# Kernel tuning notes

Hardware: AMD Instinct MI355X
Metric: run time of the kernel (lower is better)

The kernel has to match this reference:

```python
import jax, jax.numpy as jnp
import numpy as np

K = 4
TEMP = 34.0
KS = 3
PAD = 1
STRIDE = 1


def setup_inputs() -> dict:
    key = jax.random.key(0)
    k0, k1, k2, k3, k4, k5 = jax.random.split(key, 6)
    B, C, H, W = 32, 256, 56, 56
    OC = 256
    HID = int(C * 0.25) + 1  # 65
    x = jax.random.normal(k0, (B, C, H, W), jnp.float32)
    # kaiming-ish scales for the 1x1 attention convs (treated as matmuls)
    w_fc1 = jax.random.normal(k1, (HID, C), jnp.float32) * np.float32(np.sqrt(2.0 / C))
    w_fc2 = jax.random.normal(k2, (K, HID), jnp.float32) * np.float32(np.sqrt(2.0 / HID))
    b_fc2 = jnp.zeros((K,), jnp.float32)
    # positive step sizes for numerical sanity (torch inits randn then overwrites at init_state)
    alpha = jax.random.uniform(k3, (K, 1), jnp.float32, minval=0.05, maxval=1.0)
    weight = jax.random.normal(k4, (K, OC, C, KS, KS), jnp.float32) * 0.05
    bias_w = jax.random.normal(k5, (K, OC), jnp.float32) * 0.01
    return dict(x=x, w_fc1=w_fc1, w_fc2=w_fc2, b_fc2=b_fc2, alpha=alpha,
                weight=weight, bias_w=bias_w)


def _round_ste(v):
    # round_pass: forward round, backward identity
    return v + jax.lax.stop_gradient(jnp.round(v) - v)


def _lsq_quant(w2d, alpha):
    # Faithful to the torch LSQQuantizer forward (eval path): divide by per-row
    # alpha, clamp ONLY scalar elements [0,0],[1,0],[2,0] (as the torch code does),
    # then straight-through round and rescale. grad_scale copies into .data and
    # therefore has no effect on values or the autograd graph.
    d = w2d / alpha  # (K, M)
    d = d.at[0, 0].set(jnp.clip(d[0, 0], -2.0, 1.0))   # 2-bit range
    d = d.at[1, 0].set(jnp.clip(d[1, 0], -4.0, 3.0))   # 3-bit range
    d = d.at[2, 0].set(jnp.clip(d[2, 0], -8.0, 7.0))   # 4-bit range
    return _round_ste(d) * alpha


def reference(x, w_fc1, w_fc2, b_fc2, alpha, weight, bias_w):
    B, C, H, W = x.shape
    Kk, OC = bias_w.shape
    # attention2d: global avg pool -> 1x1 conv -> relu -> 1x1 conv (+bias)
    pooled = x.mean(axis=(2, 3))                     # (B, C)
    h = jax.nn.relu(pooled @ w_fc1.T)                # (B, HID)
    raw = h @ w_fc2.T + b_fc2                        # (B, K)
    # gradient_approximation: forward = one-hot(argmax), backward = softmax(x/T)
    soft = jax.nn.softmax(raw / TEMP, axis=1)
    hard = jax.nn.one_hot(jnp.argmax(raw, axis=1), Kk, dtype=raw.dtype)
    attn = soft + jax.lax.stop_gradient(hard - soft)  # (B, K)
    # LSQ-quantize flattened expert weights, then per-sample aggregation
    wq = _lsq_quant(weight.reshape(Kk, -1), alpha)   # (K, OC*C*KS*KS)
    agg_w = (attn @ wq).reshape(B, OC, C, KS, KS)    # per-sample kernels
    agg_b = attn @ bias_w                            # (B, OC)
    # per-sample conv2d (equivalent to the groups=batch trick)
    def conv1(xb, wb):
        return jax.lax.conv_general_dilated(
            xb[None], wb, (STRIDE, STRIDE), [(PAD, PAD), (PAD, PAD)],
            dimension_numbers=('NCHW', 'OIHW', 'NCHW'))[0]
    out = jax.vmap(conv1)(x, agg_w) + agg_b[:, :, None, None]  # (B, OC, H, W)
    return (out, raw)
```

## Files before the change

kernel.cpp:

```cpp
#include <hip/hip_runtime.h>
#include <hip/hip_bf16.h>

typedef __attribute__((ext_vector_type(8))) short short8;
typedef __attribute__((ext_vector_type(16))) float f32x16;

#define XPAD_OFF   0u
#define WQ_OFF     55115776u
#define POOL_OFF   59834368u
#define IDX_OFF    59867136u

__device__ __forceinline__ void gl_lds16(const void* g, void* l) {
  __builtin_amdgcn_global_load_lds(
      (const __attribute__((address_space(1))) unsigned int*)g,
      (__attribute__((address_space(3))) unsigned int*)l, 16, 0, 0);
}

__global__ __launch_bounds__(128) void fc_argmax_kernel(
    const float* __restrict__ pooled, const float* __restrict__ w_fc1,
    const float* __restrict__ w_fc2, const float* __restrict__ b_fc2,
    float* __restrict__ raw_out, int* __restrict__ idx) {
  __shared__ float h[65];
  __shared__ float raws[4];
  const int b = blockIdx.x, t = threadIdx.x;
  if (t < 65) {
    float s = 0.f;
    const float* pb = pooled + b * 256;
    const float* wr = w_fc1 + t * 256;
    for (int c = 0; c < 256; ++c) s += pb[c] * wr[c];
    s *= (1.0f / 3136.0f);
    h[t] = s > 0.f ? s : 0.f;
  }
  __syncthreads();
  if (t < 4) {
    float s = b_fc2[t];
    const float* wr = w_fc2 + t * 65;
    for (int j = 0; j < 65; ++j) s += h[j] * wr[j];
    raws[t] = s;
    raw_out[b * 4 + t] = s;
  }
  __syncthreads();
  if (t == 0) {
    int best = 0; float bv = raws[0];
    for (int k = 1; k < 4; ++k) if (raws[k] > bv) { bv = raws[k]; best = k; }
    idx[b] = best;
  }
}

__global__ __launch_bounds__(256) void quant_kernel(
    const float* __restrict__ weight, const float* __restrict__ alpha,
    __hip_bfloat16* __restrict__ Wq) {
  const unsigned d = blockIdx.x * 256u + threadIdx.x;
  const unsigned cl   = d & 7u;
  const unsigned g    = d >> 3;
  const unsigned lane = g & 63u;
  const unsigned u    = g >> 6;
  const unsigned low  = u & 63u;
  const unsigned s      = low & 1u;
  const unsigned octile = (low >> 1) & 1u;
  const unsigned wm     = (low >> 2) & 1u;
  const unsigned cbh    = (low >> 3) & 7u;
  const unsigned t6   = u >> 6;
  const unsigned tap  = t6 % 9u;
  const unsigned q    = t6 / 9u;
  const unsigned ot   = q & 1u;
  const unsigned k    = q >> 1;
  const unsigned oc = ot * 128u + wm * 64u + octile * 32u + (lane & 31u);
  const unsigned ch = cbh * 32u + s * 16u + (lane >> 5) * 8u + cl;
  const float a = alpha[k];
  float v = weight[(size_t)k * 589824u + oc * 2304u + ch * 9u + tap] / a;
  if (oc == 0u && ch == 0u && tap == 0u) {
    if (k == 0u)      v = fminf(fmaxf(v, -2.f), 1.f);
    else if (k == 1u) v = fminf(fmaxf(v, -4.f), 3.f);
    else if (k == 2u) v = fminf(fmaxf(v, -8.f), 7.f);
  }
  Wq[d] = __float2bfloat16(rintf(v) * a);
}

__global__ __launch_bounds__(256) void padx_kernel(const float* __restrict__ x,
                                                   __hip_bfloat16* __restrict__ Xpad,
                                                   float* __restrict__ pooled) {
  __shared__ float T[56 * 132];
  const int yp = blockIdx.x;
  const int c0 = blockIdx.y * 128;
  const int b  = blockIdx.z;
  const int tid = threadIdx.x;
  __hip_bfloat16* orow = Xpad + ((size_t)(b * 58 + yp) * 58) * 256 + c0;
  const short8 zero8 = (short8){0, 0, 0, 0, 0, 0, 0, 0};
  const bool rowin = (yp >= 1 && yp <= 56);
  if (rowin) {
    const float* xbase = x + (((size_t)b * 256 + c0) * 56 + (yp - 1)) * 56;
    for (int i = tid; i < 128 * 56; i += 256) {
      const int cl = i / 56, px = i - cl * 56;
      T[px * 132 + cl] = xbase[cl * 3136 + px];
    }
    __syncthreads();
    if (tid < 128) {
      float s = 0.f;
      for (int px = 0; px < 56; ++px) s += T[px * 132 + tid];
      atomicAdd(pooled + b * 256 + c0 + tid, s);
    }
    for (int i = tid; i < 896; i += 256) {
      const int px = i >> 4, cg = (i & 15) * 8;
      union { short8 v; __hip_bfloat16 e[8]; } u;
      #pragma unroll
      for (int r = 0; r < 8; ++r) u.e[r] = __float2bfloat16(T[px * 132 + cg + r]);
      *(short8*)&orow[(px + 1) * 256 + cg] = u.v;
    }
    for (int i = tid; i < 32; i += 256) {
      const int cg = (i & 15) * 8;
      const int xp = (i >> 4) ? 57 : 0;
      *(short8*)&orow[xp * 256 + cg] = zero8;
    }
  } else {
    for (int i = tid; i < 58 * 16; i += 256) {
      const int xp = i >> 4, cg = (i & 15) * 8;
      *(short8*)&orow[xp * 256 + cg] = zero8;
    }
  }
}

__global__ __launch_bounds__(256, 2) void conv_kernel(
    const __hip_bfloat16* __restrict__ Xpad, const __hip_bfloat16* __restrict__ Wq,
    const int* __restrict__ idx, const float* __restrict__ bias_w,
    float* __restrict__ out) {
  __shared__ __attribute__((aligned(16))) __hip_bfloat16 Xs[22784];

  const int tid = threadIdx.x;
  const int lane = tid & 63;
  const int w = tid >> 6;
  const int wm = w & 1;
  const int wn = w >> 1;

  const int pt = blockIdx.x;
  const int ot = blockIdx.y;
  const int b = blockIdx.z;
  const int Y0 = pt * 4;
  const int OC0 = ot * 128;
  const int kb = idx[b];

  const __hip_bfloat16* xb = Xpad + (size_t)b * (58 * 58 * 256);
  const short8* W0 = (const short8*)Wq + (size_t)(kb * 2 + ot) * 36864;

  f32x16 acc[2][4];
  #pragma unroll
  for (int i = 0; i < 2; ++i)
    #pragma unroll
    for (int j = 0; j < 4; ++j)
      acc[i][j] = (f32x16){0,0,0,0,0,0,0,0,0,0,0,0,0,0,0,0};

  const int nlo = lane & 31;
  const int khalf = lane >> 5;

  auto stageseg = [&](int cbn, int bufsel, int k) {
    int sidx = k * 64 + lane;
    int p = sidx >> 2;
    if (p > 347) p = 347;
    const int gsel = (sidx & 3) ^ ((p >> 1) & 3);
    const int r = p / 58, xc = p - r * 58;
    gl_lds16(xb + (((Y0 + r) * 58 + xc) * 256 + cbn * 32 + gsel * 8),
             (char*)Xs + bufsel * 22784 + k * 1024);
  };

  for (int k = w; k < 22; k += 4) stageseg(0, 0, k);
  __syncthreads();

  short8 afr[3][4];
  #pragma unroll
  for (int oc2 = 0; oc2 < 2; ++oc2)
    #pragma unroll
    for (int s2 = 0; s2 < 2; ++s2) {
      afr[0][oc2 * 2 + s2] = W0[0 * 4096 + 0 * 512 + wm * 256 + oc2 * 128 + s2 * 64 + lane];
      afr[1][oc2 * 2 + s2] = W0[1 * 4096 + 0 * 512 + wm * 256 + oc2 * 128 + s2 * 64 + lane];
    }

  for (int cbh = 0; cbh < 8; ++cbh) {
    const __hip_bfloat16* cur = Xs + (cbh & 1) * 11392;
    const int nb = (cbh + 1) & 1;

    #pragma unroll
    for (int t = 0; t < 9; ++t) {
      const int dy = t / 3, dx = t - dy * 3;
      if (cbh < 7) {
        if (t < 5) stageseg(cbh + 1, nb, w + 4 * t);
        else if (t == 5 && w < 2) stageseg(cbh + 1, nb, w + 20);
      }
      if (cbh < 7 || t < 7) {
        const int tap2 = (t + 2) % 9, cb2 = cbh + (t + 2) / 9;
        #pragma unroll
        for (int oc2 = 0; oc2 < 2; ++oc2)
          #pragma unroll
          for (int s2 = 0; s2 < 2; ++s2)
            afr[(t + 2) % 3][oc2 * 2 + s2] =
                W0[tap2 * 4096 + cb2 * 512 + wm * 256 + oc2 * 128 + s2 * 64 + lane];
      }
      #pragma unroll
      for (int s = 0; s < 2; ++s) {
        #pragma unroll
        for (int j = 0; j < 4; ++j) {
          const int row = wn * 2 + (j >> 1) + dy;
          const int col = (j & 1) * 32 + nlo + dx;
          const int p = row * 58 + col;
          const int slot = p * 4 + ((s * 2 + khalf) ^ ((p >> 1) & 3));
          const short8 bfr = *(const short8*)&cur[slot * 8];
          #pragma unroll
          for (int i = 0; i < 2; ++i)
            acc[i][j] = __builtin_amdgcn_mfma_f32_32x32x16_bf16(
                afr[t % 3][i * 2 + s], bfr, acc[i][j], 0, 0, 0);
        }
      }
    }
    __syncthreads();
  }

  const float* biasb = bias_w + kb * 256;
  #pragma unroll
  for (int i = 0; i < 2; ++i) {
    #pragma unroll
    for (int j = 0; j < 4; ++j) {
      const int xcol = (j & 1) * 32 + nlo;
      if (xcol < 56) {
        const int y = Y0 + wn * 2 + (j >> 1);
        #pragma unroll
        for (int reg = 0; reg < 16; ++reg) {
          const int row = (reg & 3) + 8 * (reg >> 2) + 4 * khalf;
          const int oc = OC0 + wm * 64 + i * 32 + row;
          out[(((size_t)b * 256 + oc) * 56 + y) * 56 + xcol] =
              acc[i][j][reg] + biasb[oc];
        }
      }
    }
  }
}

extern "C" void kernel_launch(void* const* d_in, const int* in_sizes, int n_in,
                              void* d_out, int out_size, void* d_ws, size_t ws_size,
                              hipStream_t stream) {
  const float* x      = (const float*)d_in[0];
  const float* w_fc1  = (const float*)d_in[1];
  const float* w_fc2  = (const float*)d_in[2];
  const float* b_fc2  = (const float*)d_in[3];
  const float* alpha  = (const float*)d_in[4];
  const float* weight = (const float*)d_in[5];
  const float* bias_w = (const float*)d_in[6];

  float* out = (float*)d_out;
  float* raw_out = out + (size_t)32 * 256 * 56 * 56;

  char* ws = (char*)d_ws;
  __hip_bfloat16* Xpad = (__hip_bfloat16*)(ws + XPAD_OFF);
  __hip_bfloat16* Wq   = (__hip_bfloat16*)(ws + WQ_OFF);
  float* pooled        = (float*)(ws + POOL_OFF);
  int* idx             = (int*)(ws + IDX_OFF);

  hipMemsetAsync(pooled, 0, 32 * 256 * sizeof(float), stream);
  padx_kernel<<<dim3(58, 2, 32), 256, 0, stream>>>(x, Xpad, pooled);
  quant_kernel<<<9216, 256, 0, stream>>>(weight, alpha, Wq);
  fc_argmax_kernel<<<32, 128, 0, stream>>>(pooled, w_fc1, w_fc2, b_fc2, raw_out, idx);
  conv_kernel<<<dim3(14, 2, 32), 256, 0, stream>>>(Xpad, Wq, idx, bias_w, out);
}
```

Baseline: 336.0 us.

## Widen conv block to 512 threads covering all output channels, vectorize pad transpose

The conv kernel now uses 8 waves per block and covers all 256 output channels, so each staged input tile in LDS is shared by twice as many channels and the input is staged half as often overall. Each wave computes a 128x64 tile (4x2 MFMA accumulators), with a 2-deep weight-fragment prefetch and compile-time buffer parity through a templated lambda. The grid is reordered with batch first. The pad/transpose kernel reads x with float4 loads and uses an LDS row stride of 133 to reduce bank conflicts. The trade-off is fewer blocks (448 instead of 896) and higher register pressure under the 512-thread launch bound.

```diff
diff --git a/kernel.cpp b/kernel.cpp
--- a/kernel.cpp
+++ b/kernel.cpp
@@ -1,5 +1,6 @@
 #include <hip/hip_runtime.h>
 #include <hip/hip_bf16.h>
+#include <type_traits>
 
 typedef __attribute__((ext_vector_type(8))) short short8;
 typedef __attribute__((ext_vector_type(16))) float f32x16;
@@ -79,7 +80,7 @@
 __global__ __launch_bounds__(256) void padx_kernel(const float* __restrict__ x,
                                                    __hip_bfloat16* __restrict__ Xpad,
                                                    float* __restrict__ pooled) {
-  __shared__ float T[56 * 132];
+  __shared__ float T[56 * 133];
   const int yp = blockIdx.x;
   const int c0 = blockIdx.y * 128;
   const int b  = blockIdx.z;
@@ -88,22 +89,24 @@
   const short8 zero8 = (short8){0, 0, 0, 0, 0, 0, 0, 0};
   const bool rowin = (yp >= 1 && yp <= 56);
   if (rowin) {
-    const float* xbase = x + (((size_t)b * 256 + c0) * 56 + (yp - 1)) * 56;
-    for (int i = tid; i < 128 * 56; i += 256) {
-      const int cl = i / 56, px = i - cl * 56;
-      T[px * 132 + cl] = xbase[cl * 3136 + px];
+    const float4* xb4 = (const float4*)(x + (((size_t)b * 256 + c0) * 56 + (yp - 1)) * 56);
+    for (int i = tid; i < 1792; i += 256) {
+      const int cl = i / 14, p4 = i - cl * 14;
+      const float4 v = xb4[(size_t)cl * 784 + p4];
+      float* Tp = &T[(p4 * 4) * 133 + cl];
+      Tp[0] = v.x; Tp[133] = v.y; Tp[266] = v.z; Tp[399] = v.w;
     }
     __syncthreads();
     if (tid < 128) {
       float s = 0.f;
-      for (int px = 0; px < 56; ++px) s += T[px * 132 + tid];
+      for (int px = 0; px < 56; ++px) s += T[px * 133 + tid];
       atomicAdd(pooled + b * 256 + c0 + tid, s);
     }
     for (int i = tid; i < 896; i += 256) {
       const int px = i >> 4, cg = (i & 15) * 8;
       union { short8 v; __hip_bfloat16 e[8]; } u;
       #pragma unroll
-      for (int r = 0; r < 8; ++r) u.e[r] = __float2bfloat16(T[px * 132 + cg + r]);
+      for (int r = 0; r < 8; ++r) u.e[r] = __float2bfloat16(T[px * 133 + cg + r]);
       *(short8*)&orow[(px + 1) * 256 + cg] = u.v;
     }
     for (int i = tid; i < 32; i += 256) {
@@ -119,7 +122,7 @@
   }
 }
 
-__global__ __launch_bounds__(256, 2) void conv_kernel(
+__global__ __launch_bounds__(512, 2) void conv_kernel(
     const __hip_bfloat16* __restrict__ Xpad, const __hip_bfloat16* __restrict__ Wq,
     const int* __restrict__ idx, const float* __restrict__ bias_w,
     float* __restrict__ out) {
@@ -128,24 +131,22 @@
   const int tid = threadIdx.x;
   const int lane = tid & 63;
   const int w = tid >> 6;
-  const int wm = w & 1;
-  const int wn = w >> 1;
-
-  const int pt = blockIdx.x;
-  const int ot = blockIdx.y;
-  const int b = blockIdx.z;
+  const int wn = w & 3;
+  const int wm = w >> 2;
+
+  const int b  = blockIdx.x;
+  const int pt = blockIdx.y;
   const int Y0 = pt * 4;
-  const int OC0 = ot * 128;
   const int kb = idx[b];
 
   const __hip_bfloat16* xb = Xpad + (size_t)b * (58 * 58 * 256);
-  const short8* W0 = (const short8*)Wq + (size_t)(kb * 2 + ot) * 36864;
-
-  f32x16 acc[2][4];
+  const short8* Wk = (const short8*)Wq + (size_t)(kb * 2 + wm) * 36864;
+
+  f32x16 acc[4][2];
   #pragma unroll
-  for (int i = 0; i < 2; ++i)
+  for (int i = 0; i < 4; ++i)
     #pragma unroll
-    for (int j = 0; j < 4; ++j)
+    for (int j = 0; j < 2; ++j)
       acc[i][j] = (f32x16){0,0,0,0,0,0,0,0,0,0,0,0,0,0,0,0};
 
   const int nlo = lane & 31;
@@ -161,69 +162,73 @@
              (char*)Xs + bufsel * 22784 + k * 1024);
   };
 
-  for (int k = w; k < 22; k += 4) stageseg(0, 0, k);
+  for (int k = w; k < 22; k += 8) stageseg(0, 0, k);
   __syncthreads();
 
-  short8 afr[3][4];
+  short8 afr[2][8];
   #pragma unroll
-  for (int oc2 = 0; oc2 < 2; ++oc2)
+  for (int i2 = 0; i2 < 4; ++i2)
     #pragma unroll
-    for (int s2 = 0; s2 < 2; ++s2) {
-      afr[0][oc2 * 2 + s2] = W0[0 * 4096 + 0 * 512 + wm * 256 + oc2 * 128 + s2 * 64 + lane];
-      afr[1][oc2 * 2 + s2] = W0[1 * 4096 + 0 * 512 + wm * 256 + oc2 * 128 + s2 * 64 + lane];
-    }
-
-  for (int cbh = 0; cbh < 8; ++cbh) {
-    const __hip_bfloat16* cur = Xs + (cbh & 1) * 11392;
-    const int nb = (cbh + 1) & 1;
-
+    for (int s2 = 0; s2 < 2; ++s2)
+      afr[0][i2 * 2 + s2] = Wk[(i2 >> 1) * 256 + (i2 & 1) * 128 + s2 * 64 + lane];
+
+  auto chunk = [&](int cbh, auto parc) {
+    constexpr int PAR = decltype(parc)::value;
+    const __hip_bfloat16* cur = Xs + PAR * 11392;
+    const int nb = PAR ^ 1;
     #pragma unroll
     for (int t = 0; t < 9; ++t) {
       const int dy = t / 3, dx = t - dy * 3;
       if (cbh < 7) {
-        if (t < 5) stageseg(cbh + 1, nb, w + 4 * t);
-        else if (t == 5 && w < 2) stageseg(cbh + 1, nb, w + 20);
-      }
-      if (cbh < 7 || t < 7) {
-        const int tap2 = (t + 2) % 9, cb2 = cbh + (t + 2) / 9;
+        if (t < 2) stageseg(cbh + 1, nb, w + 8 * t);
+        else if (t == 2 && w < 6) stageseg(cbh + 1, nb, w + 16);
+      }
+      if (cbh < 7 || t < 8) {
+        const int tap2 = (t + 1) % 9, cb2 = cbh + (t + 1) / 9;
         #pragma unroll
-        for (int oc2 = 0; oc2 < 2; ++oc2)
+        for (int i2 = 0; i2 < 4; ++i2)
           #pragma unroll
           for (int s2 = 0; s2 < 2; ++s2)
-            afr[(t + 2) % 3][oc2 * 2 + s2] =
-                W0[tap2 * 4096 + cb2 * 512 + wm * 256 + oc2 * 128 + s2 * 64 + lane];
+            afr[(t + 1 + PAR) & 1][i2 * 2 + s2] =
+                Wk[tap2 * 4096 + cb2 * 512 + (i2 >> 1) * 256 + (i2 & 1) * 128 +
+                   s2 * 64 + lane];
       }
       #pragma unroll
       for (int s = 0; s < 2; ++s) {
         #pragma unroll
-        for (int j = 0; j < 4; ++j) {
-          const int row = wn * 2 + (j >> 1) + dy;
-          const int col = (j & 1) * 32 + nlo + dx;
+        for (int j = 0; j < 2; ++j) {
+          const int row = wn + dy;
+          const int col = j * 32 + nlo + dx;
           const int p = row * 58 + col;
           const int slot = p * 4 + ((s * 2 + khalf) ^ ((p >> 1) & 3));
           const short8 bfr = *(const short8*)&cur[slot * 8];
           #pragma unroll
-          for (int i = 0; i < 2; ++i)
+          for (int i = 0; i < 4; ++i)
             acc[i][j] = __builtin_amdgcn_mfma_f32_32x32x16_bf16(
-                afr[t % 3][i * 2 + s], bfr, acc[i][j], 0, 0, 0);
+                afr[(t + PAR) & 1][i * 2 + s], bfr, acc[i][j], 0, 0, 0);
         }
       }
     }
     __syncthreads();
+  };
+
+  for (int c2 = 0; c2 < 8; c2 += 2) {
+    chunk(c2,     std::integral_constant<int, 0>{});
+    chunk(c2 + 1, std::integral_constant<int, 1>{});
   }
 
   const float* biasb = bias_w + kb * 256;
+  const int y = Y0 + wn;
   #pragma unroll
-  for (int i = 0; i < 2; ++i) {
-    #pragma unroll
-    for (int j = 0; j < 4; ++j) {
-      const int xcol = (j & 1) * 32 + nlo;
-      if (xcol < 56) {
-        const int y = Y0 + wn * 2 + (j >> 1);
+  for (int j = 0; j < 2; ++j) {
+    const int xcol = j * 32 + nlo;
+    if (xcol < 56) {
+      #pragma unroll
+      for (int i = 0; i < 4; ++i) {
         #pragma unroll
         for (int reg = 0; reg < 16; ++reg) {
-          const int row = (reg & 3) + 8 * (reg >> 2) + 4 * khalf;
-          const int oc = OC0 + wm * 64 + i * 32 + row;
+          const int rowr = (reg & 3) + 8 * (reg >> 2) + 4 * khalf;
+          const int oc = wm * 128 + i * 32 + rowr;
           out[(((size_t)b * 256 + oc) * 56 + y) * 56 + xcol] =
               acc[i][j][reg] + biasb[oc];
         }
@@ -256,5 +261,5 @@
   padx_kernel<<<dim3(58, 2, 32), 256, 0, stream>>>(x, Xpad, pooled);
   quant_kernel<<<9216, 256, 0, stream>>>(weight, alpha, Wq);
   fc_argmax_kernel<<<32, 128, 0, stream>>>(pooled, w_fc1, w_fc2, b_fc2, raw_out, idx);
-  conv_kernel<<<dim3(14, 2, 32), 256, 0, stream>>>(Xpad, Wq, idx, bias_w, out);
-}
+  conv_kernel<<<dim3(32, 14), 512, 0, stream>>>(Xpad, Wq, idx, bias_w, out);
+}
```

Result: slower. 373.2 us (+11.1%).
